# Performance work log

Measured on AMD Instinct MI355X. Metric: run time of the kernel, lower is better.

Reference implementation:

```python
import jax, jax.numpy as jnp
import numpy as np

N_NODES = 100000
N_EDGES = 1600000
NODE_F = 8   # augmented node features
EDGE_F = 2   # augmented edge features
GLOB_F = 1
HID = 16
L = 3        # message passing steps

EDGE_IN = GLOB_F + EDGE_F + 2 * NODE_F   # 19
NODE_IN = GLOB_F + EDGE_F + NODE_F       # 11
GLOB_IN = EDGE_F + NODE_F + GLOB_F       # 11


def setup_inputs() -> dict:
    key = jax.random.key(0)
    ks = jax.random.split(key, 20)
    inp = {
        "x": jax.random.normal(ks[0], (N_NODES, NODE_F), dtype=jnp.float32),
        "edge_index": jax.random.randint(ks[1], (2, N_EDGES), 0, N_NODES, dtype=jnp.int32),
        "edge_attr": jax.random.normal(ks[2], (N_EDGES, EDGE_F), dtype=jnp.float32),
        "g": jax.random.normal(ks[3], (1, GLOB_F), dtype=jnp.float32),
    }
    s = 0.1
    inp["edge_W1"] = jax.random.normal(ks[4], (L, EDGE_IN, HID), dtype=jnp.float32) * s
    inp["edge_b1"] = jnp.zeros((L, HID), dtype=jnp.float32)
    inp["edge_W2"] = jax.random.normal(ks[5], (L, HID, EDGE_F), dtype=jnp.float32) * s
    inp["edge_b2"] = jnp.zeros((L, EDGE_F), dtype=jnp.float32)
    inp["node_W1"] = jax.random.normal(ks[6], (L, NODE_IN, HID), dtype=jnp.float32) * s
    inp["node_b1"] = jnp.zeros((L, HID), dtype=jnp.float32)
    inp["node_W2"] = jax.random.normal(ks[7], (L, HID, NODE_F), dtype=jnp.float32) * s
    inp["node_b2"] = jnp.zeros((L, NODE_F), dtype=jnp.float32)
    inp["glob_W1"] = jax.random.normal(ks[8], (L, GLOB_IN, HID), dtype=jnp.float32) * s
    inp["glob_b1"] = jnp.zeros((L, HID), dtype=jnp.float32)
    inp["glob_W2"] = jax.random.normal(ks[9], (L, HID, GLOB_F), dtype=jnp.float32) * s
    inp["glob_b2"] = jnp.zeros((L, GLOB_F), dtype=jnp.float32)
    return inp


def _mlp(h, W1, b1, W2, b2):
    # two-layer MLP with ReLU after first layer only (activate_final=False, no layer_norm)
    return jnp.maximum(h @ W1 + b1, 0.0) @ W2 + b2


def reference(x, edge_index, edge_attr, g,
              edge_W1, edge_b1, edge_W2, edge_b2,
              node_W1, node_b1, node_W2, node_b2,
              glob_W1, glob_b1, glob_W2, glob_b2):
    row, col = edge_index[0], edge_index[1]
    n = x.shape[0]
    for l in range(L):
        g_e = jnp.broadcast_to(g, (row.shape[0], GLOB_F))
        # edge block: gather node features along edges, concat, MLP -> [E, EDGE_F]
        e_in = jnp.concatenate([g_e, x[row], x[col], edge_attr], axis=1)
        edge_emb = _mlp(e_in, edge_W1[l], edge_b1[l], edge_W2[l], edge_b2[l])
        # sum-aggregate edge embeddings to source nodes
        agg = jax.ops.segment_sum(edge_emb, row, num_segments=n)
        g_n = jnp.broadcast_to(g, (n, GLOB_F))
        node_emb = _mlp(jnp.concatenate([g_n, x, agg], axis=1),
                        node_W1[l], node_b1[l], node_W2[l], node_b2[l])
        # global block on mean-aggregated edge/node embeddings
        edge_gl = jnp.mean(edge_emb, axis=0, keepdims=True)
        node_gl = jnp.mean(node_emb, axis=0, keepdims=True)
        g = _mlp(jnp.concatenate([node_gl, edge_gl, g], axis=1),
                 glob_W1[l], glob_b1[l], glob_W2[l], glob_b2[l])
        x, edge_attr = node_emb, edge_emb
    return x  # final node embeddings [N, NODE_F]
```

## Files before the change

### kernel.cpp

```cpp
#include <hip/hip_runtime.h>

#define NN 100000
#define NE 1600000
#define SCAN_B 1024
#define NBLK_SCAN ((NN + SCAN_B - 1) / SCAN_B)

__device__ __forceinline__ float wave_red(float v) {
#pragma unroll
    for (int off = 32; off > 0; off >>= 1) v += __shfl_down(v, off, 64);
    return v;
}

__global__ __launch_bounds__(256) void build1_kernel(
    const int* __restrict__ ei, int* __restrict__ cnt, int* __restrict__ posArr)
{
    int e = blockIdx.x * 256 + threadIdx.x;
    if (e < NE) posArr[e] = atomicAdd(&cnt[ei[e]], 1);
}

__global__ __launch_bounds__(SCAN_B) void scan1_kernel(
    const int* __restrict__ cnt, int* __restrict__ bsum)
{
    int i = blockIdx.x * SCAN_B + threadIdx.x;
    int v = (i < NN) ? cnt[i] : 0;
#pragma unroll
    for (int off = 32; off > 0; off >>= 1) v += __shfl_down(v, off, 64);
    __shared__ int wsum[16];
    int wave = threadIdx.x >> 6, lane = threadIdx.x & 63;
    if (lane == 0) wsum[wave] = v;
    __syncthreads();
    if (threadIdx.x == 0) {
        int s = 0;
#pragma unroll
        for (int w = 0; w < 16; w++) s += wsum[w];
        bsum[blockIdx.x] = s;
    }
}

__global__ __launch_bounds__(SCAN_B) void scan3_kernel(
    const int* cnt, const int* __restrict__ bsum, int* off)
{
    __shared__ int sarr[NBLK_SCAN];
    __shared__ int sbase;
    int t = threadIdx.x;
    if (t < NBLK_SCAN) sarr[t] = bsum[t];
    __syncthreads();
    if (t == 0) {
        int s = 0;
        for (int b = 0; b < (int)blockIdx.x; b++) s += sarr[b];
        sbase = s;
    }

    __shared__ int buf[2][SCAN_B];
    int i = blockIdx.x * SCAN_B + t;
    int v = (i < NN) ? cnt[i] : 0;
    buf[0][t] = v;
    __syncthreads();
    int src = 0;
    for (int d = 1; d < SCAN_B; d <<= 1) {
        int nv = buf[src][t] + ((t >= d) ? buf[src][t - d] : 0);
        buf[src ^ 1][t] = nv;
        src ^= 1;
        __syncthreads();
    }
    if (i < NN) off[i] = sbase + buf[src][t] - v;
    if (blockIdx.x == NBLK_SCAN - 1 && t == SCAN_B - 1)
        off[NN] = sbase + buf[src][t];
}

__global__ __launch_bounds__(256) void fill2_kernel(
    const int* __restrict__ ei, const int* __restrict__ posArr,
    const int* __restrict__ off, const float* __restrict__ eattr,
    float4* __restrict__ rec)
{
    int e = blockIdx.x * 256 + threadIdx.x;
    if (e < NE) {
        int row = ei[e];
        int j = off[row] + posArr[e];
        float2 ea = reinterpret_cast<const float2*>(eattr)[e];
        float4 v;
        v.x = __int_as_float(row);
        v.y = __int_as_float(ei[NE + e]);
        v.z = ea.x; v.w = ea.y;
        rec[j] = v;
    }
}

__global__ __launch_bounds__(256) void prep_kernel(
    const float* __restrict__ x, const float* __restrict__ W1,
    float* __restrict__ Pr, float* __restrict__ Pc)
{
    int i = blockIdx.x * 256 + threadIdx.x;
    if (i >= NN) return;
    const float4* xi = reinterpret_cast<const float4*>(x + (size_t)i * 8);
    float4 a0 = xi[0], a1 = xi[1];
    float xv[8] = {a0.x, a0.y, a0.z, a0.w, a1.x, a1.y, a1.z, a1.w};
    float pr[16], pc[16];
#pragma unroll
    for (int q = 0; q < 16; q++) { pr[q] = 0.f; pc[q] = 0.f; }
#pragma unroll
    for (int k = 0; k < 8; k++) {
        float v = xv[k];
#pragma unroll
        for (int q = 0; q < 16; q++) {
            pr[q] += v * W1[(1 + k) * 16 + q];
            pc[q] += v * W1[(9 + k) * 16 + q];
        }
    }
    float4* po = reinterpret_cast<float4*>(Pr + (size_t)i * 16);
#pragma unroll
    for (int t = 0; t < 4; t++)
        po[t] = make_float4(pr[4 * t], pr[4 * t + 1], pr[4 * t + 2], pr[4 * t + 3]);
    float4* qo = reinterpret_cast<float4*>(Pc + (size_t)i * 16);
#pragma unroll
    for (int t = 0; t < 4; t++)
        qo[t] = make_float4(pc[4 * t], pc[4 * t + 1], pc[4 * t + 2], pc[4 * t + 3]);
}

template <bool WRITE_REC, bool NEED_SUM, bool HAS_NEXT>
__global__ __launch_bounds__(256, 4) void fused_kernel(
    float4* __restrict__ rec, const int* __restrict__ off,
    const float* __restrict__ PrIn, const float* __restrict__ PcIn,
    const float* __restrict__ gptr,
    const float* __restrict__ eW1, const float* __restrict__ eB1,
    const float* __restrict__ eW2, const float* __restrict__ eB2,
    const float* __restrict__ x,
    const float* __restrict__ nW1, const float* __restrict__ nB1,
    const float* __restrict__ nW2, const float* __restrict__ nB2,
    const float* __restrict__ nextW1,
    float* __restrict__ PrOut, float* __restrict__ PcOut,
    float* __restrict__ xout, float* __restrict__ sums)
{
    __shared__ float sagg[256][2];
    __shared__ float redE[4][2];
    __shared__ float redN[4][8];
    int tid = threadIdx.x;
    sagg[tid][0] = 0.f; sagg[tid][1] = 0.f;
    __syncthreads();

    int n0 = blockIdx.x * 256;
    int nEnd = n0 + 256; if (nEnd > NN) nEnd = NN;
    int e0 = off[n0], e1 = off[nEnd];

    float gval = gptr[0];
    float gterm[16];
#pragma unroll
    for (int q = 0; q < 16; q++) gterm[q] = eB1[q] + gval * eW1[q];

    float t0 = 0.f, t1 = 0.f;
    for (int e = e0 + tid; e < e1; e += 256) {
        float4 r = rec[e];
        int row = __float_as_int(r.x);
        int col = __float_as_int(r.y);
        float ea0 = r.z, ea1 = r.w;
        const float4* pr = reinterpret_cast<const float4*>(PrIn + (size_t)row * 16);
        const float4* pc = reinterpret_cast<const float4*>(PcIn + (size_t)col * 16);
        float4 r0 = pr[0], r1 = pr[1], r2 = pr[2], r3 = pr[3];
        float4 c0 = pc[0], c1 = pc[1], c2 = pc[2], c3 = pc[3];
        float h[16];
        h[0]  = gterm[0]  + r0.x + c0.x;
        h[1]  = gterm[1]  + r0.y + c0.y;
        h[2]  = gterm[2]  + r0.z + c0.z;
        h[3]  = gterm[3]  + r0.w + c0.w;
        h[4]  = gterm[4]  + r1.x + c1.x;
        h[5]  = gterm[5]  + r1.y + c1.y;
        h[6]  = gterm[6]  + r1.z + c1.z;
        h[7]  = gterm[7]  + r1.w + c1.w;
        h[8]  = gterm[8]  + r2.x + c2.x;
        h[9]  = gterm[9]  + r2.y + c2.y;
        h[10] = gterm[10] + r2.z + c2.z;
        h[11] = gterm[11] + r2.w + c2.w;
        h[12] = gterm[12] + r3.x + c3.x;
        h[13] = gterm[13] + r3.y + c3.y;
        h[14] = gterm[14] + r3.z + c3.z;
        h[15] = gterm[15] + r3.w + c3.w;
#pragma unroll
        for (int q = 0; q < 16; q++) {
            h[q] += ea0 * eW1[17 * 16 + q];
            h[q] += ea1 * eW1[18 * 16 + q];
        }
        float s0 = eB2[0], s1 = eB2[1];
#pragma unroll
        for (int q = 0; q < 16; q++) {
            float rr = fmaxf(h[q], 0.f);
            s0 += rr * eW2[2 * q];
            s1 += rr * eW2[2 * q + 1];
        }
        if (WRITE_REC) {
            float4 w;
            w.x = r.x; w.y = r.y; w.z = s0; w.w = s1;
            rec[e] = w;
        }
        int li = row - n0;
        atomicAdd(&sagg[li][0], s0);
        atomicAdd(&sagg[li][1], s1);
        t0 += s0; t1 += s1;
    }

    if (NEED_SUM) {
        float r0 = wave_red(t0);
        float r1 = wave_red(t1);
        int wave = tid >> 6, lane = tid & 63;
        if (lane == 0) { redE[wave][0] = r0; redE[wave][1] = r1; }
    }
    __syncthreads();
    if (NEED_SUM && tid == 0) {
        atomicAdd(&sums[0], redE[0][0] + redE[1][0] + redE[2][0] + redE[3][0]);
        atomicAdd(&sums[1], redE[0][1] + redE[1][1] + redE[2][1] + redE[3][1]);
    }

    int n = n0 + tid;
    float out[8];
#pragma unroll
    for (int m = 0; m < 8; m++) out[m] = 0.f;

    if (n < NN) {
        float in[11];
        in[0] = gval;
        const float4* xi = reinterpret_cast<const float4*>(x + (size_t)n * 8);
        float4 a0 = xi[0], a1 = xi[1];
        in[1] = a0.x; in[2] = a0.y; in[3] = a0.z; in[4] = a0.w;
        in[5] = a1.x; in[6] = a1.y; in[7] = a1.z; in[8] = a1.w;
        in[9] = sagg[tid][0]; in[10] = sagg[tid][1];

        float h[16];
#pragma unroll
        for (int q = 0; q < 16; q++) h[q] = nB1[q];
#pragma unroll
        for (int k = 0; k < 11; k++) {
            float v = in[k];
#pragma unroll
            for (int q = 0; q < 16; q++) h[q] += v * nW1[k * 16 + q];
        }
#pragma unroll
        for (int m = 0; m < 8; m++) out[m] = nB2[m];
#pragma unroll
        for (int q = 0; q < 16; q++) {
            float hq = fmaxf(h[q], 0.f);
#pragma unroll
            for (int m = 0; m < 8; m++) out[m] += hq * nW2[q * 8 + m];
        }
        float4* xo = reinterpret_cast<float4*>(xout + (size_t)n * 8);
        xo[0] = make_float4(out[0], out[1], out[2], out[3]);
        xo[1] = make_float4(out[4], out[5], out[6], out[7]);

        if (HAS_NEXT) {
            float pr[16], pc[16];
#pragma unroll
            for (int q = 0; q < 16; q++) { pr[q] = 0.f; pc[q] = 0.f; }
#pragma unroll
            for (int k = 0; k < 8; k++) {
                float v = out[k];
#pragma unroll
                for (int q = 0; q < 16; q++) {
                    pr[q] += v * nextW1[(1 + k) * 16 + q];
                    pc[q] += v * nextW1[(9 + k) * 16 + q];
                }
            }
            float4* po = reinterpret_cast<float4*>(PrOut + (size_t)n * 16);
#pragma unroll
            for (int t = 0; t < 4; t++)
                po[t] = make_float4(pr[4*t], pr[4*t+1], pr[4*t+2], pr[4*t+3]);
            float4* qo = reinterpret_cast<float4*>(PcOut + (size_t)n * 16);
#pragma unroll
            for (int t = 0; t < 4; t++)
                qo[t] = make_float4(pc[4*t], pc[4*t+1], pc[4*t+2], pc[4*t+3]);
        }
    }
    if (NEED_SUM) {
        float r[8];
#pragma unroll
        for (int m = 0; m < 8; m++) r[m] = wave_red(out[m]);
        int wave = tid >> 6, lane = tid & 63;
        if (lane == 0) {
#pragma unroll
            for (int m = 0; m < 8; m++) redN[wave][m] = r[m];
        }
        __syncthreads();
        if (tid == 0) {
#pragma unroll
            for (int m = 0; m < 8; m++) {
                float s = redN[0][m] + redN[1][m] + redN[2][m] + redN[3][m];
                atomicAdd(&sums[2 + m], s);
            }
        }
    }
}

__global__ void glob_kernel(const float* __restrict__ sums,
                            const float* __restrict__ gold,
                            const float* __restrict__ W1, const float* __restrict__ B1,
                            const float* __restrict__ W2, const float* __restrict__ B2,
                            float* __restrict__ gnew)
{
    if (threadIdx.x == 0 && blockIdx.x == 0) {
        float in[11];
#pragma unroll
        for (int j = 0; j < 8; j++) in[j] = sums[2 + j] * (1.0f / NN);
        in[8] = sums[0] * (1.0f / NE);
        in[9] = sums[1] * (1.0f / NE);
        in[10] = gold[0];
        float acc = B2[0];
#pragma unroll
        for (int j = 0; j < 16; j++) {
            float h = B1[j];
#pragma unroll
            for (int k = 0; k < 11; k++) h += in[k] * W1[k * 16 + j];
            acc += fmaxf(h, 0.f) * W2[j];
        }
        gnew[0] = acc;
    }
}

extern "C" void kernel_launch(void* const* d_in, const int* in_sizes, int n_in,
                              void* d_out, int out_size, void* d_ws, size_t ws_size,
                              hipStream_t stream) {
    const float* x     = (const float*)d_in[0];
    const int*   ei    = (const int*)d_in[1];
    const float* eattr = (const float*)d_in[2];
    const float* g     = (const float*)d_in[3];
    const float* eW1 = (const float*)d_in[4];
    const float* eB1 = (const float*)d_in[5];
    const float* eW2 = (const float*)d_in[6];
    const float* eB2 = (const float*)d_in[7];
    const float* nW1 = (const float*)d_in[8];
    const float* nB1 = (const float*)d_in[9];
    const float* nW2 = (const float*)d_in[10];
    const float* nB2 = (const float*)d_in[11];
    const float* gW1 = (const float*)d_in[12];
    const float* gB1 = (const float*)d_in[13];
    const float* gW2 = (const float*)d_in[14];
    const float* gB2 = (const float*)d_in[15];
    float* out = (float*)d_out;

    char* ws = (char*)d_ws;
    float*  xb0    = (float*)(ws);
    int*    off    = (int*)  (ws + 3200000);
    int*    cnt    = off;
    int*    bsum   = (int*)  (ws + 3600064);
    float*  sums   = (float*)(ws + 3600512);
    float*  g1     = (float*)(ws + 3600640);
    float*  g2     = g1 + 1;
    float4* rec    = (float4*)(ws + 3600704);
    float*  PrA    = (float*)(ws + 29200704);
    float*  PcA    = (float*)(ws + 35600704);
    float*  PrB    = (float*)(ws + 42000704);
    int*    posArr = (int*)  PrB;
    float*  PcB    = (float*)(ws + 48400704);
    float*  xb1    = out;

    dim3 blk(256);
    dim3 egrid(NE / 256);
    dim3 ngrid((NN + 255) / 256);

    hipMemsetAsync(cnt, 0, 400000, stream);
    hipMemsetAsync(sums, 0, 192, stream);
    build1_kernel<<<egrid, blk, 0, stream>>>(ei, cnt, posArr);
    scan1_kernel<<<NBLK_SCAN, SCAN_B, 0, stream>>>(cnt, bsum);
    scan3_kernel<<<NBLK_SCAN, SCAN_B, 0, stream>>>(cnt, bsum, off);
    fill2_kernel<<<egrid, blk, 0, stream>>>(ei, posArr, off, eattr, rec);
    prep_kernel<<<ngrid, blk, 0, stream>>>(x, eW1, PrA, PcA);

    fused_kernel<true, true, true><<<ngrid, blk, 0, stream>>>(
        rec, off, PrA, PcA, g,
        eW1, eB1, eW2, eB2,
        x, nW1, nB1, nW2, nB2,
        eW1 + 304, PrB, PcB, xb0, sums);
    glob_kernel<<<1, 64, 0, stream>>>(sums, g, gW1, gB1, gW2, gB2, g1);

    fused_kernel<true, true, true><<<ngrid, blk, 0, stream>>>(
        rec, off, PrB, PcB, g1,
        eW1 + 304, eB1 + 16, eW2 + 32, eB2 + 2,
        xb0, nW1 + 176, nB1 + 16, nW2 + 128, nB2 + 8,
        eW1 + 608, PrA, PcA, xb1, sums + 16);
    glob_kernel<<<1, 64, 0, stream>>>(sums + 16, g1, gW1 + 176, gB1 + 16, gW2 + 16, gB2 + 1, g2);

    fused_kernel<false, false, false><<<ngrid, blk, 0, stream>>>(
        rec, off, PrA, PcA, g2,
        eW1 + 608, eB1 + 32, eW2 + 64, eB2 + 4,
        xb1, nW1 + 352, nB1 + 32, nW2 + 256, nB2 + 16,
        nullptr, nullptr, nullptr, out, sums);
}
```

Baseline: 399.6 us.

## Replace per-node CSR sort with bucketed counting sort by 256-node blocks

```diff
diff --git a/kernel.cpp b/kernel.cpp
--- a/kernel.cpp
+++ b/kernel.cpp
@@ -2,8 +2,9 @@
 
 #define NN 100000
 #define NE 1600000
-#define SCAN_B 1024
-#define NBLK_SCAN ((NN + SCAN_B - 1) / SCAN_B)
+#define CH 4096
+#define NCHUNK ((NE + CH - 1) / CH)
+#define NBUCK ((NN + 255) / 256)
 
 __device__ __forceinline__ float wave_red(float v) {
 #pragma unroll
@@ -11,78 +12,83 @@
     return v;
 }
 
-__global__ __launch_bounds__(256) void build1_kernel(
-    const int* __restrict__ ei, int* __restrict__ cnt, int* __restrict__ posArr)
-{
-    int e = blockIdx.x * 256 + threadIdx.x;
-    if (e < NE) posArr[e] = atomicAdd(&cnt[ei[e]], 1);
-}
-
-__global__ __launch_bounds__(SCAN_B) void scan1_kernel(
-    const int* __restrict__ cnt, int* __restrict__ bsum)
-{
-    int i = blockIdx.x * SCAN_B + threadIdx.x;
-    int v = (i < NN) ? cnt[i] : 0;
-#pragma unroll
-    for (int off = 32; off > 0; off >>= 1) v += __shfl_down(v, off, 64);
-    __shared__ int wsum[16];
-    int wave = threadIdx.x >> 6, lane = threadIdx.x & 63;
-    if (lane == 0) wsum[wave] = v;
-    __syncthreads();
-    if (threadIdx.x == 0) {
-        int s = 0;
-#pragma unroll
-        for (int w = 0; w < 16; w++) s += wsum[w];
-        bsum[blockIdx.x] = s;
-    }
-}
-
-__global__ __launch_bounds__(SCAN_B) void scan3_kernel(
-    const int* cnt, const int* __restrict__ bsum, int* off)
-{
-    __shared__ int sarr[NBLK_SCAN];
-    __shared__ int sbase;
-    int t = threadIdx.x;
-    if (t < NBLK_SCAN) sarr[t] = bsum[t];
-    __syncthreads();
-    if (t == 0) {
-        int s = 0;
-        for (int b = 0; b < (int)blockIdx.x; b++) s += sarr[b];
-        sbase = s;
-    }
-
-    __shared__ int buf[2][SCAN_B];
-    int i = blockIdx.x * SCAN_B + t;
-    int v = (i < NN) ? cnt[i] : 0;
+__global__ __launch_bounds__(256) void hist_kernel(
+    const int* __restrict__ ei, int* __restrict__ hist)
+{
+    __shared__ int h[NBUCK];
+    int t = threadIdx.x, c = blockIdx.x;
+    for (int b = t; b < NBUCK; b += 256) h[b] = 0;
+    __syncthreads();
+    int base = c * CH;
+    for (int i = t; i < CH; i += 256) {
+        int e = base + i;
+        if (e < NE) atomicAdd(&h[ei[e] >> 8], 1);
+    }
+    __syncthreads();
+    for (int b = t; b < NBUCK; b += 256) hist[c * NBUCK + b] = h[b];
+}
+
+__global__ __launch_bounds__(512) void bscan_kernel(
+    const int* __restrict__ hist, int* __restrict__ baseT, int* __restrict__ colTotal)
+{
+    __shared__ int buf[2][512];
+    int b = blockIdx.x, t = threadIdx.x;
+    int v = (t < NCHUNK) ? hist[t * NBUCK + b] : 0;
     buf[0][t] = v;
     __syncthreads();
     int src = 0;
-    for (int d = 1; d < SCAN_B; d <<= 1) {
+    for (int d = 1; d < 512; d <<= 1) {
         int nv = buf[src][t] + ((t >= d) ? buf[src][t - d] : 0);
         buf[src ^ 1][t] = nv;
         src ^= 1;
         __syncthreads();
     }
-    if (i < NN) off[i] = sbase + buf[src][t] - v;
-    if (blockIdx.x == NBLK_SCAN - 1 && t == SCAN_B - 1)
-        off[NN] = sbase + buf[src][t];
-}
-
-__global__ __launch_bounds__(256) void fill2_kernel(
-    const int* __restrict__ ei, const int* __restrict__ posArr,
-    const int* __restrict__ off, const float* __restrict__ eattr,
+    if (t < NCHUNK) baseT[b * NCHUNK + t] = buf[src][t] - v;
+    if (t == NCHUNK - 1) colTotal[b] = buf[src][t];
+}
+
+__global__ __launch_bounds__(512) void boff_kernel(
+    const int* __restrict__ colTotal, int* __restrict__ b_off)
+{
+    __shared__ int buf[2][512];
+    int t = threadIdx.x;
+    int v = (t < NBUCK) ? colTotal[t] : 0;
+    buf[0][t] = v;
+    __syncthreads();
+    int src = 0;
+    for (int d = 1; d < 512; d <<= 1) {
+        int nv = buf[src][t] + ((t >= d) ? buf[src][t - d] : 0);
+        buf[src ^ 1][t] = nv;
+        src ^= 1;
+        __syncthreads();
+    }
+    if (t < NBUCK) b_off[t] = buf[src][t] - v;
+    if (t == NBUCK - 1) b_off[NBUCK] = buf[src][t];
+}
+
+__global__ __launch_bounds__(256) void fillb_kernel(
+    const int* __restrict__ ei, const float* __restrict__ eattr,
+    const int* __restrict__ baseT, const int* __restrict__ b_off,
     float4* __restrict__ rec)
 {
-    int e = blockIdx.x * 256 + threadIdx.x;
-    if (e < NE) {
-        int row = ei[e];
-        int j = off[row] + posArr[e];
-        float2 ea = reinterpret_cast<const float2*>(eattr)[e];
-        float4 v;
-        v.x = __int_as_float(row);
-        v.y = __int_as_float(ei[NE + e]);
-        v.z = ea.x; v.w = ea.y;
-        rec[j] = v;
+    __shared__ int sslot[NBUCK];
+    int t = threadIdx.x, c = blockIdx.x;
+    for (int b = t; b < NBUCK; b += 256)
+        sslot[b] = b_off[b] + baseT[b * NCHUNK + c];
+    __syncthreads();
+    int base = c * CH;
+    for (int i = t; i < CH; i += 256) {
+        int e = base + i;
+        if (e < NE) {
+            int row = ei[e];
+            int slot = atomicAdd(&sslot[row >> 8], 1);
+            float2 ea = reinterpret_cast<const float2*>(eattr)[e];
+            float4 v;
+            v.x = __int_as_float(row);
+            v.y = __int_as_float(ei[NE + e]);
+            v.z = ea.x; v.w = ea.y;
+            rec[slot] = v;
+        }
     }
 }
 
@@ -119,7 +125,7 @@
 
 template <bool WRITE_REC, bool NEED_SUM, bool HAS_NEXT>
 __global__ __launch_bounds__(256, 4) void fused_kernel(
-    float4* __restrict__ rec, const int* __restrict__ off,
+    float4* __restrict__ rec, const int* __restrict__ b_off,
     const float* __restrict__ PrIn, const float* __restrict__ PcIn,
     const float* __restrict__ gptr,
     const float* __restrict__ eW1, const float* __restrict__ eB1,
@@ -139,8 +145,7 @@
     __syncthreads();
 
     int n0 = blockIdx.x * 256;
-    int nEnd = n0 + 256; if (nEnd > NN) nEnd = NN;
-    int e0 = off[n0], e1 = off[nEnd];
+    int e0 = b_off[blockIdx.x], e1 = b_off[blockIdx.x + 1];
 
     float gval = gptr[0];
     float gterm[16];
@@ -335,49 +340,48 @@
 
     char* ws = (char*)d_ws;
     float*  xb0    = (float*)(ws);
-    int*    off    = (int*)  (ws + 3200000);
-    int*    cnt    = off;
-    int*    bsum   = (int*)  (ws + 3600064);
-    float*  sums   = (float*)(ws + 3600512);
-    float*  g1     = (float*)(ws + 3600640);
+    int*    b_off  = (int*)  (ws + 3200000);
+    float*  sums   = (float*)(ws + 3201600);
+    float*  g1     = (float*)(ws + 3201728);
     float*  g2     = g1 + 1;
-    float4* rec    = (float4*)(ws + 3600704);
-    float*  PrA    = (float*)(ws + 29200704);
-    float*  PcA    = (float*)(ws + 35600704);
-    float*  PrB    = (float*)(ws + 42000704);
-    int*    posArr = (int*)  PrB;
-    float*  PcB    = (float*)(ws + 48400704);
-    float*  xb1    = out;
+    float4* rec    = (float4*)(ws + 3201792);
+    float*  PrA    = (float*)(ws + 28801792);
+    float*  PcA    = (float*)(ws + 35201792);
+    float*  PrB    = (float*)(ws + 41601792);
+    float*  PcB    = (float*)(ws + 48001792);
+    int*    hist     = (int*)PrB;
+    int*    baseT    = (int*)((char*)PrB + 611584);
+    int*    colTotal = (int*)((char*)PrB + 1223168);
 
     dim3 blk(256);
-    dim3 egrid(NE / 256);
+    dim3 cgrid(NCHUNK);
+    dim3 bgrid(NBUCK);
     dim3 ngrid((NN + 255) / 256);
 
-    hipMemsetAsync(cnt, 0, 400000, stream);
     hipMemsetAsync(sums, 0, 192, stream);
-    build1_kernel<<<egrid, blk, 0, stream>>>(ei, cnt, posArr);
-    scan1_kernel<<<NBLK_SCAN, SCAN_B, 0, stream>>>(cnt, bsum);
-    scan3_kernel<<<NBLK_SCAN, SCAN_B, 0, stream>>>(cnt, bsum, off);
-    fill2_kernel<<<egrid, blk, 0, stream>>>(ei, posArr, off, eattr, rec);
+    hist_kernel<<<cgrid, blk, 0, stream>>>(ei, hist);
+    bscan_kernel<<<bgrid, 512, 0, stream>>>(hist, baseT, colTotal);
+    boff_kernel<<<1, 512, 0, stream>>>(colTotal, b_off);
+    fillb_kernel<<<cgrid, blk, 0, stream>>>(ei, eattr, baseT, b_off, rec);
     prep_kernel<<<ngrid, blk, 0, stream>>>(x, eW1, PrA, PcA);
 
-    fused_kernel<true, true, true><<<ngrid, blk, 0, stream>>>(
-        rec, off, PrA, PcA, g,
+    fused_kernel<true, true, true><<<bgrid, blk, 0, stream>>>(
+        rec, b_off, PrA, PcA, g,
         eW1, eB1, eW2, eB2,
         x, nW1, nB1, nW2, nB2,
         eW1 + 304, PrB, PcB, xb0, sums);
     glob_kernel<<<1, 64, 0, stream>>>(sums, g, gW1, gB1, gW2, gB2, g1);
 
-    fused_kernel<true, true, true><<<ngrid, blk, 0, stream>>>(
-        rec, off, PrB, PcB, g1,
+    fused_kernel<true, true, true><<<bgrid, blk, 0, stream>>>(
+        rec, b_off, PrB, PcB, g1,
         eW1 + 304, eB1 + 16, eW2 + 32, eB2 + 2,
         xb0, nW1 + 176, nB1 + 16, nW2 + 128, nB2 + 8,
-        eW1 + 608, PrA, PcA, xb1, sums + 16);
+        eW1 + 608, PrA, PcA, (float*)out, sums + 16);
     glob_kernel<<<1, 64, 0, stream>>>(sums + 16, g1, gW1 + 176, gB1 + 16, gW2 + 16, gB2 + 1, g2);
 
-    fused_kernel<false, false, false><<<ngrid, blk, 0, stream>>>(
-        rec, off, PrA, PcA, g2,
+    fused_kernel<false, false, false><<<bgrid, blk, 0, stream>>>(
+        rec, b_off, PrA, PcA, g2,
         eW1 + 608, eB1 + 32, eW2 + 64, eB2 + 4,
-        xb1, nW1 + 352, nB1 + 32, nW2 + 256, nB2 + 16,
+        (float*)out, nW1 + 352, nB1 + 32, nW2 + 256, nB2 + 16,
         nullptr, nullptr, nullptr, out, sums);
 }
```

New measurement: 370.3 us. 7.3% less time.
